# Kernel optimization log

Measured on AMD Instinct MI355X. Metric: run time of the kernel, lower is better.

## Reference

```python
import jax, jax.numpy as jnp
import numpy as np

G = (1.0, 1.0)  # Clifford signature g = [1, 1]
MODES1 = 32
MODES2 = 32


def _clifford_kernel_2d(w, g):
    # w: (4, O, Cin, 2*m1, 2*m2); returns (4*O, 4*Cin, 2*m1, 2*m2)
    g0, g1 = g
    k0 = jnp.concatenate([w[0], g0 * w[1], g1 * w[2], -g0 * g1 * w[3]], axis=1)
    k1 = jnp.concatenate([w[1], w[0], -g1 * w[3], g1 * w[2]], axis=1)
    k2 = jnp.concatenate([w[2], g0 * w[3], w[0], -g0 * w[1]], axis=1)
    k3 = jnp.concatenate([w[3], w[2], -w[1], w[0]], axis=1)
    return jnp.concatenate([k0, k1, k2, k3], axis=0)


def _forward(x, weights):
    # x: (B, C, H, W, 4) multivector field
    B, C, H, W, I = x.shape
    m1, m2 = MODES1, MODES2
    # dual-pair complexification: (scalar, e12) and (e1, e2)
    d1 = jax.lax.complex(x[..., 0], x[..., 3])
    d2 = jax.lax.complex(x[..., 1], x[..., 2])
    d1f = jnp.fft.fft2(d1)  # over last two axes (H, W)
    d2f = jnp.fft.fft2(d2)
    # stacked blades in Fourier space: (B, 4*C, H, W)
    mv = jnp.concatenate([d1f.real, d2f.real, d2f.imag, d1f.imag], axis=1)
    # crop low-frequency corner modes into a (2*m1, 2*m2) block
    top = jnp.concatenate([mv[:, :, :m1, :m2], mv[:, :, :m1, -m2:]], axis=-1)
    bot = jnp.concatenate([mv[:, :, -m1:, :m2], mv[:, :, -m1:, -m2:]], axis=-1)
    inp = jnp.concatenate([top, bot], axis=-2)  # (B, 4*C, 2*m1, 2*m2)
    kernel = _clifford_kernel_2d(weights, G)  # (4*O, 4*C, 2*m1, 2*m2)
    out = jnp.einsum('bixy,oixy->boxy', inp, kernel)  # geometric-product mode mix
    O4 = kernel.shape[0]
    # scatter the four corners back into a zero-padded full spectrum
    out_ft = jnp.zeros((B, O4, H, W), dtype=x.dtype)
    out_ft = out_ft.at[:, :, :m1, :m2].set(out[:, :, :m1, :m2])
    out_ft = out_ft.at[:, :, -m1:, :m2].set(out[:, :, -m1:, :m2])
    out_ft = out_ft.at[:, :, :m1, -m2:].set(out[:, :, :m1, -m2:])
    out_ft = out_ft.at[:, :, -m1:, -m2:].set(out[:, :, -m1:, -m2:])
    # (B, 4, O, H, W) -> (B, O, H, W, 4)
    out_ft = out_ft.reshape(B, 4, O4 // 4, H, W).transpose(0, 2, 3, 4, 1)
    od1 = jax.lax.complex(out_ft[..., 0], out_ft[..., 3])
    od2 = jax.lax.complex(out_ft[..., 1], out_ft[..., 2])
    o1 = jnp.fft.ifft2(od1)
    o2 = jnp.fft.ifft2(od2)
    return jnp.stack([o1.real, o2.real, o2.imag, o1.imag], axis=-1)


def setup_inputs() -> dict:
    key = jax.random.key(0)
    kx, kw = jax.random.split(key)
    B, Cin, Cout, H, W = 4, 32, 32, 256, 256
    x = jax.random.normal(kx, (B, Cin, H, W, 4), dtype=jnp.float32)
    scale = 1.0 / (Cin * Cout)
    weights = scale * jax.random.uniform(kw, (4, Cout, Cin, 2 * MODES1, 2 * MODES2), dtype=jnp.float32)
    return {"x": x, "weights": weights}


def reference(x, weights):
    return _forward(x, weights)
```

## Files before the change

### kernel.cpp

```cpp
#include <hip/hip_runtime.h>
#include <hip/hip_fp16.h>
#include <math.h>

#define TWO_PI 6.28318530717958647692f

__device__ __forceinline__ void cmac(float2& a, const float2 b, const float2 c) {
  a.x = fmaf(b.x, c.x, fmaf(-b.y, c.y, a.x));
  a.y = fmaf(b.x, c.y, fmaf(b.y, c.x, a.y));
}
__device__ __forceinline__ __half2 pkh(const float xx, const float yy) {
  return __floats2half2_rn(xx, yy);
}
__device__ __forceinline__ float2 uph(const __half2 h) { return __half22float2(h); }

#define FMA4(a, b, v)                 \
  {                                   \
    a.x = fmaf(b.x, v.x, a.x);        \
    a.y = fmaf(b.y, v.y, a.y);        \
    a.z = fmaf(b.z, v.z, a.z);        \
    a.w = fmaf(b.w, v.w, a.w);        \
  }
#define FMS4(a, b, v)                 \
  {                                   \
    a.x = fmaf(-b.x, v.x, a.x);       \
    a.y = fmaf(-b.y, v.y, a.y);       \
    a.z = fmaf(-b.z, v.z, a.z);       \
    a.w = fmaf(-b.w, v.w, a.w);       \
  }

#define W16_C {1.f, 0.92387953f, 0.70710678f, 0.38268343f, 0.f, -0.38268343f, -0.70710678f, -0.92387953f, -1.f, -0.92387953f, -0.70710678f, -0.38268343f, 0.f, 0.38268343f, 0.70710678f, 0.92387953f}
#define W16_S {0.f, 0.38268343f, 0.70710678f, 0.92387953f, 1.f, 0.92387953f, 0.70710678f, 0.38268343f, 0.f, -0.38268343f, -0.70710678f, -0.92387953f, -1.f, -0.92387953f, -0.70710678f, -0.38268343f}

__device__ __forceinline__ void idft16_p1(const float2* a, const int p1,
                                          float2* X) {
  const float WC[16] = W16_C;
  const float WS[16] = W16_S;
  float2 tt[4];
#pragma unroll
  for (int r1 = 0; r1 < 4; ++r1) {
    const float2 q0 = a[r1], q1 = a[r1 + 4], q2 = a[r1 + 8], q3 = a[r1 + 12];
    const float2 s = make_float2(q0.x + q2.x, q0.y + q2.y);
    const float2 d = make_float2(q0.x - q2.x, q0.y - q2.y);
    const float2 u = make_float2(q1.x + q3.x, q1.y + q3.y);
    const float2 e = make_float2(q1.x - q3.x, q1.y - q3.y);
    float2 in;
    if (p1 == 0)      in = make_float2(s.x + u.x, s.y + u.y);
    else if (p1 == 1) in = make_float2(d.x - e.y, d.y + e.x);
    else if (p1 == 2) in = make_float2(s.x - u.x, s.y - u.y);
    else              in = make_float2(d.x + e.y, d.y - e.x);
    const float wc = WC[(r1 * p1) & 15], ws = WS[(r1 * p1) & 15];
    tt[r1] = make_float2(fmaf(in.x, wc, -in.y * ws), fmaf(in.y, wc, in.x * ws));
  }
  const float2 s = make_float2(tt[0].x + tt[2].x, tt[0].y + tt[2].y);
  const float2 d = make_float2(tt[0].x - tt[2].x, tt[0].y - tt[2].y);
  const float2 u = make_float2(tt[1].x + tt[3].x, tt[1].y + tt[3].y);
  const float2 e = make_float2(tt[1].x - tt[3].x, tt[1].y - tt[3].y);
  X[0] = make_float2(s.x + u.x, s.y + u.y);
  X[1] = make_float2(d.x - e.y, d.y + e.x);
  X[2] = make_float2(s.x - u.x, s.y - u.y);
  X[3] = make_float2(d.x + e.y, d.y - e.x);
}

__global__ __launch_bounds__(512) void f1_dft_h(const float* __restrict__ x,
                                                __half2* __restrict__ G) {
  __shared__ float2 twn[256];
  __shared__ __align__(16) __half2 yf[64][4][17][2];
  const int t = threadIdx.x;
  if (t < 256) {
    float sv, cv;
    sincosf(-TWO_PI * (float)t * (1.0f / 256.0f), &sv, &cv);
    twn[t] = make_float2(cv, sv);
  }
  const int bid = blockIdx.x;
  const int img = bid >> 4;
  const int w0  = (bid & 15) << 4;
  const float4* __restrict__ xb = (const float4*)x + (size_t)img * 65536 + w0;
#pragma unroll
  for (int i = 0; i < 2; ++i) {
    const int idxs = t + (i << 9);
    const int n1 = idxs >> 4, wl = idxs & 15;
    const float4 v0 = xb[(size_t)(n1)*256 + wl];
    const float4 v1 = xb[(size_t)(n1 + 64) * 256 + wl];
    const float4 v2 = xb[(size_t)(n1 + 128) * 256 + wl];
    const float4 v3 = xb[(size_t)(n1 + 192) * 256 + wl];
    {
      const float sx = v0.x + v2.x, sy = v0.w + v2.w;
      const float dx = v0.x - v2.x, dy = v0.w - v2.w;
      const float ux = v1.x + v3.x, uy = v1.w + v3.w;
      const float ex = v1.x - v3.x, ey = v1.w - v3.w;
      yf[n1][0][wl][0] = pkh(sx + ux, sy + uy);
      yf[n1][2][wl][0] = pkh(sx - ux, sy - uy);
      yf[n1][1][wl][0] = pkh(dx + ey, dy - ex);
      yf[n1][3][wl][0] = pkh(dx - ey, dy + ex);
    }
    {
      const float sx = v0.y + v2.y, sy = v0.z + v2.z;
      const float dx = v0.y - v2.y, dy = v0.z - v2.z;
      const float ux = v1.y + v3.y, uy = v1.z + v3.z;
      const float ex = v1.y - v3.y, ey = v1.z - v3.z;
      yf[n1][0][wl][1] = pkh(sx + ux, sy + uy);
      yf[n1][2][wl][1] = pkh(sx - ux, sy - uy);
      yf[n1][1][wl][1] = pkh(dx + ey, dy - ex);
      yf[n1][3][wl][1] = pkh(dx - ey, dy + ex);
    }
  }
  __syncthreads();
  const int wl   = t & 15;
  const int dual = (t >> 4) & 1;
  const int kb   = t >> 5;
  const int r    = kb & 3;
  float2 a[16];
#pragma unroll
  for (int c = 0; c < 16; ++c) a[c] = make_float2(0.f, 0.f);
  int idx = 0;
#pragma unroll
  for (int n1 = 0; n1 < 64; ++n1) {
    const float2 tv = twn[idx];
    const float2 yv = uph(yf[n1][r][wl][dual]);
    cmac(a[n1 & 15], yv, tv);
    idx = (idx + kb) & 255;
  }
  const float WC[16] = W16_C;
  const float WS[16] = W16_S;
  float2 D0 = make_float2(0.f, 0.f), D1 = D0, D2 = D0, D3 = D0;
#pragma unroll
  for (int c = 0; c < 16; ++c) {
    const float2 av = a[c];
    const float cc = WC[c], ss = WS[c];
    const float cc2 = WC[(2 * c) & 15], ss2 = WS[(2 * c) & 15];
    D0.x += av.x;                        D0.y += av.y;
    D1.x = fmaf(av.x, cc,  fmaf( av.y, ss,  D1.x));
    D1.y = fmaf(av.y, cc,  fmaf(-av.x, ss,  D1.y));
    D2.x = fmaf(av.x, cc2, fmaf(-av.y, ss2, D2.x));
    D2.y = fmaf(av.y, cc2, fmaf( av.x, ss2, D2.y));
    D3.x = fmaf(av.x, cc,  fmaf(-av.y, ss,  D3.x));
    D3.y = fmaf(av.y, cc,  fmaf( av.x, ss,  D3.y));
  }
  __syncthreads();
  __half2(*dl)[64][16] = reinterpret_cast<__half2(*)[64][16]>(&yf[0][0][0][0]);
  dl[dual][kb][wl]      = pkh(D0.x, D0.y);
  dl[dual][kb + 16][wl] = pkh(D1.x, D1.y);
  dl[dual][kb + 32][wl] = pkh(D2.x, D2.y);
  dl[dual][kb + 48][wl] = pkh(D3.x, D3.y);
  __syncthreads();
  const __half2* __restrict__ dfl = &dl[0][0][0];
  const int flat = t << 2;
  const int wq = flat & 15, kx = (flat >> 4) & 63, dd = flat >> 10;
  const size_t row = (size_t)(img * 2 + dd) * 64 + kx;
  *reinterpret_cast<float4*>(&G[row * 256 + w0 + wq]) =
      *reinterpret_cast<const float4*>(&dfl[flat]);
}

__global__ __launch_bounds__(256) void f2_dft_w(const __half2* __restrict__ G,
                                                __half2* __restrict__ mi) {
  __shared__ float2 twn[256];
  __shared__ float2 yf[16][65][4];
  const int t = threadIdx.x;
  {
    float sv, cv;
    sincosf(-TWO_PI * (float)t * (1.0f / 256.0f), &sv, &cv);
    twn[t] = make_float2(cv, sv);
  }
  const int row0 = blockIdx.x * 16;
  for (int idx = t; idx < 1024; idx += 256) {
    const int tr = idx >> 6, n1 = idx & 63;
    const __half2* __restrict__ Gp = G + (size_t)(row0 + tr) * 256;
    const float2 z0 = uph(Gp[n1]), z1 = uph(Gp[n1 + 64]);
    const float2 z2 = uph(Gp[n1 + 128]), z3 = uph(Gp[n1 + 192]);
    const float sx = z0.x + z2.x, sy = z0.y + z2.y;
    const float dx = z0.x - z2.x, dy = z0.y - z2.y;
    const float ux = z1.x + z3.x, uy = z1.y + z3.y;
    const float ex = z1.x - z3.x, ey = z1.y - z3.y;
    yf[tr][n1][0] = make_float2(sx + ux, sy + uy);
    yf[tr][n1][2] = make_float2(sx - ux, sy - uy);
    yf[tr][n1][1] = make_float2(dx + ey, dy - ex);
    yf[tr][n1][3] = make_float2(dx - ey, dy + ex);
  }
  __syncthreads();
  const int kslot = t & 15;
  const int trow  = t >> 4;
  const int r     = kslot & 3;
  float2 acc[16];
#pragma unroll
  for (int c = 0; c < 16; ++c) acc[c] = make_float2(0.f, 0.f);
  int idx = 0;
#pragma unroll
  for (int n1 = 0; n1 < 64; ++n1) {
    const float2 tv = twn[idx];
    const float2 yv = yf[trow][n1][r];
    cmac(acc[n1 & 15], yv, tv);
    idx = (idx + kslot) & 255;
  }
  const float WC[16] = W16_C;
  const float WS[16] = W16_S;
  float2 D[4];
  D[0] = make_float2(0.f, 0.f); D[1] = D[0]; D[2] = D[0]; D[3] = D[0];
#pragma unroll
  for (int c = 0; c < 16; ++c) {
    const float2 a = acc[c];
    const float cc = WC[c], ss = WS[c];
    const float cc2 = WC[(2 * c) & 15], ss2 = WS[(2 * c) & 15];
    D[0].x += a.x;                        D[0].y += a.y;
    D[1].x = fmaf(a.x, cc,  fmaf( a.y, ss,  D[1].x));
    D[1].y = fmaf(a.y, cc,  fmaf(-a.x, ss,  D[1].y));
    D[2].x = fmaf(a.x, cc2, fmaf(-a.y, ss2, D[2].x));
    D[2].y = fmaf(a.y, cc2, fmaf( a.x, ss2, D[2].y));
    D[3].x = fmaf(a.x, cc,  fmaf(-a.y, ss,  D[3].x));
    D[3].y = fmaf(a.y, cc,  fmaf( a.x, ss,  D[3].y));
  }
  const int row  = row0 + trow;
  const int kx   = row & 63;
  const int dual = (row >> 6) & 1;
  const int bc   = row >> 7;
  const int b = bc >> 5, cc = bc & 31;
#pragma unroll
  for (int m = 0; m < 4; ++m) {
    const int kyi = kslot + (m << 4);
    mi[((size_t)((b * 2 + dual) * 32 + cc)) * 4096 + kx * 64 + kyi] =
        pkh(D[m].x, D[m].y);
  }
}

__global__ __launch_bounds__(256) void ein_k(const __half2* __restrict__ mi,
                                             const float* __restrict__ wgt,
                                             __half2* __restrict__ mo) {
  __shared__ float si[4][128][16];
  const int t = threadIdx.x;
  const int bid = blockIdx.x;
  const int m0 = (bid >> 1) << 4;
  const int oh = bid & 1;
  for (int idx = t; idx < 4096; idx += 256) {
    const int q = idx & 15, c = (idx >> 4) & 31, dual = (idx >> 9) & 1, b = idx >> 10;
    const float2 f = uph(mi[((size_t)((b * 2 + dual) * 32 + c)) * 4096 + m0 + q]);
    if (dual == 0) { si[b][c][q] = f.x;      si[b][96 + c][q] = f.y; }
    else           { si[b][32 + c][q] = f.x; si[b][64 + c][q] = f.y; }
  }
  __syncthreads();
  const int qv  = t & 3;
  const int o16 = (t >> 2) & 15;
  const int b   = t >> 6;
  const int o   = oh * 16 + o16;
  const int q0  = qv << 2;
  const float* __restrict__ wb = wgt + (size_t)o * 131072 + m0 + q0;
  float4 acc[4];
#pragma unroll
  for (int r = 0; r < 4; ++r) acc[r] = make_float4(0.f, 0.f, 0.f, 0.f);
  float4 wA[4], wB[4];
#pragma unroll
  for (int j = 0; j < 4; ++j)
    wA[j] = *reinterpret_cast<const float4*>(&wb[(size_t)j * 4194304]);
#pragma unroll
  for (int j = 0; j < 4; ++j)
    wB[j] = *reinterpret_cast<const float4*>(&wb[(size_t)j * 4194304 + 4096]);
#pragma unroll 1
  for (int c = 0; c < 32; ++c) {
    float4 wv[4];
#pragma unroll
    for (int j = 0; j < 4; ++j) { wv[j] = wA[j]; wA[j] = wB[j]; }
    if (c + 2 < 32) {
#pragma unroll
      for (int j = 0; j < 4; ++j)
        wB[j] = *reinterpret_cast<const float4*>(
            &wb[(size_t)j * 4194304 + (size_t)(c + 2) * 4096]);
    }
    const float4 iv0 = *reinterpret_cast<const float4*>(&si[b][c][q0]);
    const float4 iv1 = *reinterpret_cast<const float4*>(&si[b][32 + c][q0]);
    const float4 iv2 = *reinterpret_cast<const float4*>(&si[b][64 + c][q0]);
    const float4 iv3 = *reinterpret_cast<const float4*>(&si[b][96 + c][q0]);
    FMA4(acc[0], wv[0], iv0); FMA4(acc[0], wv[1], iv1);
    FMA4(acc[0], wv[2], iv2); FMS4(acc[0], wv[3], iv3);
    FMA4(acc[1], wv[1], iv0); FMA4(acc[1], wv[0], iv1);
    FMS4(acc[1], wv[3], iv2); FMA4(acc[1], wv[2], iv3);
    FMA4(acc[2], wv[2], iv0); FMA4(acc[2], wv[3], iv1);
    FMA4(acc[2], wv[0], iv2); FMS4(acc[2], wv[1], iv3);
    FMA4(acc[3], wv[3], iv0); FMA4(acc[3], wv[2], iv1);
    FMS4(acc[3], wv[1], iv2); FMA4(acc[3], wv[0], iv3);
  }
  __half2 h0[4], h1[4];
  h0[0] = pkh(acc[0].x, acc[3].x); h0[1] = pkh(acc[0].y, acc[3].y);
  h0[2] = pkh(acc[0].z, acc[3].z); h0[3] = pkh(acc[0].w, acc[3].w);
  h1[0] = pkh(acc[1].x, acc[2].x); h1[1] = pkh(acc[1].y, acc[2].y);
  h1[2] = pkh(acc[1].z, acc[2].z); h1[3] = pkh(acc[1].w, acc[2].w);
  *reinterpret_cast<float4*>(&mo[((size_t)((b * 2 + 0) * 32 + o)) * 4096 + m0 + q0]) =
      *reinterpret_cast<const float4*>(h0);
  *reinterpret_cast<float4*>(&mo[((size_t)((b * 2 + 1) * 32 + o)) * 4096 + m0 + q0]) =
      *reinterpret_cast<const float4*>(h1);
}

__global__ __launch_bounds__(256) void i1_idft_w(const __half2* __restrict__ mo,
                                                 __half2* __restrict__ T) {
  __shared__ float2 twc[256];
  __shared__ float2 srow[16][66];
  const int t = threadIdx.x;
  {
    float sv, cv;
    sincosf(TWO_PI * (float)t * (1.0f / 256.0f), &sv, &cv);
    twc[t] = make_float2(cv, sv);
  }
  const int row0 = blockIdx.x * 16;
  for (int idx = t; idx < 1024; idx += 256) {
    const int tr = idx >> 6, ky = idx & 63;
    const int row = row0 + tr;
    const int kx = row & 63;
    const int dual = (row >> 6) & 1;
    const int bo = row >> 7;
    const int b = bo >> 5, o = bo & 31;
    srow[tr][ky] =
        uph(mo[((size_t)((b * 2 + dual) * 32 + o)) * 4096 + kx * 64 + ky]);
  }
  __syncthreads();
  const int n1   = t & 15;
  const int trow = t >> 4;
  float2 a[16];
#pragma unroll
  for (int c = 0; c < 16; ++c) a[c] = make_float2(0.f, 0.f);
  int idx = 0;
#pragma unroll
  for (int kyi = 0; kyi < 64; ++kyi) {
    if (kyi == 32) idx = (idx + 192 * n1) & 255;
    cmac(a[kyi & 15], srow[trow][kyi], twc[idx]);
    idx = (idx + n1) & 255;
  }
  const int row = row0 + trow;
  __half2* __restrict__ Tp = T + (size_t)row * 256;
#pragma unroll
  for (int p1 = 0; p1 < 4; ++p1) {
    float2 X[4];
    idft16_p1(a, p1, X);
#pragma unroll
    for (int p2 = 0; p2 < 4; ++p2)
      Tp[n1 + 16 * (p1 + 4 * p2)] = pkh(X[p2].x, X[p2].y);
  }
}

__global__ __launch_bounds__(256) void i2_idft_h(const __half2* __restrict__ T,
                                                 float* __restrict__ out) {
  __shared__ float2 twc[256];
  __shared__ float2 Tl[2][64][16];
  const int t = threadIdx.x;
  {
    float sv, cv;
    sincosf(TWO_PI * (float)t * (1.0f / 256.0f), &sv, &cv);
    twc[t] = make_float2(cv, sv);
  }
  const int bid = blockIdx.x;
  const int bo = bid >> 4;
  const int w0 = (bid & 15) << 4;
  const __half2* __restrict__ Tp = T + (size_t)bo * 32768;
  for (int idx = t; idx < 2048; idx += 256) {
    const int ww = idx & 15, kxi = (idx >> 4) & 63, dual = idx >> 10;
    Tl[dual][kxi][ww] = uph(Tp[((size_t)dual * 64 + kxi) * 256 + w0 + ww]);
  }
  __syncthreads();
  const int wl = t & 15;
  const int n1 = t >> 4;
  float2 a0[16], a1[16];
#pragma unroll
  for (int c = 0; c < 16; ++c) {
    a0[c] = make_float2(0.f, 0.f);
    a1[c] = make_float2(0.f, 0.f);
  }
  int idx = 0;
#pragma unroll
  for (int kxi = 0; kxi < 64; ++kxi) {
    if (kxi == 32) idx = (idx + 192 * n1) & 255;
    const float2 tv = twc[idx];
    cmac(a0[kxi & 15], Tl[0][kxi][wl], tv);
    cmac(a1[kxi & 15], Tl[1][kxi][wl], tv);
    idx = (idx + n1) & 255;
  }
  const float sc = 1.0f / 65536.0f;
  float4* __restrict__ op = (float4*)out + (size_t)bo * 65536 + w0 + wl;
#pragma unroll
  for (int p1 = 0; p1 < 4; ++p1) {
    float2 X0[4], X1[4];
    idft16_p1(a0, p1, X0);
    idft16_p1(a1, p1, X1);
#pragma unroll
    for (int p2 = 0; p2 < 4; ++p2) {
      const int h = n1 + 16 * (p1 + 4 * p2);
      op[(size_t)h * 256] = make_float4(X0[p2].x * sc, X1[p2].x * sc,
                                        X1[p2].y * sc, X0[p2].y * sc);
    }
  }
}

extern "C" void kernel_launch(void* const* d_in, const int* in_sizes, int n_in,
                              void* d_out, int out_size, void* d_ws, size_t ws_size,
                              hipStream_t stream) {
  const float* x = (const float*)d_in[0];
  const float* wgt = (const float*)d_in[1];
  float* out = (float*)d_out;
  __half2* G  = (__half2*)d_ws;
  __half2* mi = G + 4194304;
  __half2* mo = mi + 1048576;

  hipLaunchKernelGGL(f1_dft_h, dim3(2048), dim3(512), 0, stream, x, G);
  hipLaunchKernelGGL(f2_dft_w, dim3(1024), dim3(256), 0, stream, G, mi);
  hipLaunchKernelGGL(ein_k,    dim3(512),  dim3(256), 0, stream, mi, wgt, mo);
  hipLaunchKernelGGL(i1_idft_w, dim3(1024), dim3(256), 0, stream, mo, G);
  hipLaunchKernelGGL(i2_idft_h, dim3(2048), dim3(256), 0, stream, G, out);
}
```

Baseline: 128.8 us.

## Split einsum over input channels so each weight load serves all batches

The mode-mixing kernel previously gave each thread one batch and all 32 input channels, so every weight was loaded from global memory four times, once per batch thread. Now each thread handles all four batches for a slice of 8 input channels, which cuts weight traffic fourfold. The partial sums are then combined through a shared-memory tree reduction. In exchange it uses 64 accumulator registers per thread, adds a large shared reduction buffer that lowers occupancy, and adds several barriers.

Measured after the change: 138.1 us. 1.07x slower.

```diff
diff --git a/kernel.cpp b/kernel.cpp
--- a/kernel.cpp
+++ b/kernel.cpp
@@ -59,6 +59,27 @@
   X[1] = make_float2(d.x - e.y, d.y + e.x);
   X[2] = make_float2(s.x - u.x, s.y - u.y);
   X[3] = make_float2(d.x + e.y, d.y - e.x);
+}
+
+__device__ __forceinline__ void clif_c(const float4 w[4],
+                                       const float (*si)[128][16],
+                                       const int c, const int q0,
+                                       float4 (*acc)[4]) {
+#pragma unroll
+  for (int b = 0; b < 4; ++b) {
+    const float4 iv0 = *reinterpret_cast<const float4*>(&si[b][c][q0]);
+    const float4 iv1 = *reinterpret_cast<const float4*>(&si[b][32 + c][q0]);
+    const float4 iv2 = *reinterpret_cast<const float4*>(&si[b][64 + c][q0]);
+    const float4 iv3 = *reinterpret_cast<const float4*>(&si[b][96 + c][q0]);
+    FMA4(acc[b][0], w[0], iv0); FMA4(acc[b][0], w[1], iv1);
+    FMA4(acc[b][0], w[2], iv2); FMS4(acc[b][0], w[3], iv3);
+    FMA4(acc[b][1], w[1], iv0); FMA4(acc[b][1], w[0], iv1);
+    FMS4(acc[b][1], w[3], iv2); FMA4(acc[b][1], w[2], iv3);
+    FMA4(acc[b][2], w[2], iv0); FMA4(acc[b][2], w[3], iv1);
+    FMA4(acc[b][2], w[0], iv2); FMS4(acc[b][2], w[1], iv3);
+    FMA4(acc[b][3], w[3], iv0); FMA4(acc[b][3], w[2], iv1);
+    FMS4(acc[b][3], w[1], iv2); FMA4(acc[b][3], w[0], iv3);
+  }
 }
 
 __global__ __launch_bounds__(512) void f1_dft_h(const float* __restrict__ x,
@@ -225,6 +246,7 @@
                                              const float* __restrict__ wgt,
                                              __half2* __restrict__ mo) {
   __shared__ float si[4][128][16];
+  __shared__ float red[128 * 65];
   const int t = threadIdx.x;
   const int bid = blockIdx.x;
   const int m0 = (bid >> 1) << 4;
@@ -236,55 +258,110 @@
     else           { si[b][32 + c][q] = f.x; si[b][64 + c][q] = f.y; }
   }
   __syncthreads();
-  const int qv  = t & 3;
+  const int qv = t & 3;
   const int o16 = (t >> 2) & 15;
-  const int b   = t >> 6;
-  const int o   = oh * 16 + o16;
-  const int q0  = qv << 2;
+  const int cs = t >> 6;
+  const int o = oh * 16 + o16;
+  const int q0 = qv << 2;
+  const int c0 = cs << 3;
   const float* __restrict__ wb = wgt + (size_t)o * 131072 + m0 + q0;
-  float4 acc[4];
-#pragma unroll
-  for (int r = 0; r < 4; ++r) acc[r] = make_float4(0.f, 0.f, 0.f, 0.f);
-  float4 wA[4], wB[4];
+  float4 acc[4][4];
+#pragma unroll
+  for (int b = 0; b < 4; ++b)
+#pragma unroll
+    for (int r = 0; r < 4; ++r) acc[b][r] = make_float4(0.f, 0.f, 0.f, 0.f);
+  float4 wE[4], wO[4];
 #pragma unroll
   for (int j = 0; j < 4; ++j)
-    wA[j] = *reinterpret_cast<const float4*>(&wb[(size_t)j * 4194304]);
+    wE[j] = *reinterpret_cast<const float4*>(&wb[(size_t)j * 4194304 + (size_t)c0 * 4096]);
 #pragma unroll
   for (int j = 0; j < 4; ++j)
-    wB[j] = *reinterpret_cast<const float4*>(&wb[(size_t)j * 4194304 + 4096]);
+    wO[j] = *reinterpret_cast<const float4*>(&wb[(size_t)j * 4194304 + (size_t)(c0 + 1) * 4096]);
 #pragma unroll 1
-  for (int c = 0; c < 32; ++c) {
-    float4 wv[4];
-#pragma unroll
-    for (int j = 0; j < 4; ++j) { wv[j] = wA[j]; wA[j] = wB[j]; }
-    if (c + 2 < 32) {
-#pragma unroll
-      for (int j = 0; j < 4; ++j)
-        wB[j] = *reinterpret_cast<const float4*>(
-            &wb[(size_t)j * 4194304 + (size_t)(c + 2) * 4096]);
-    }
-    const float4 iv0 = *reinterpret_cast<const float4*>(&si[b][c][q0]);
-    const float4 iv1 = *reinterpret_cast<const float4*>(&si[b][32 + c][q0]);
-    const float4 iv2 = *reinterpret_cast<const float4*>(&si[b][64 + c][q0]);
-    const float4 iv3 = *reinterpret_cast<const float4*>(&si[b][96 + c][q0]);
-    FMA4(acc[0], wv[0], iv0); FMA4(acc[0], wv[1], iv1);
-    FMA4(acc[0], wv[2], iv2); FMS4(acc[0], wv[3], iv3);
-    FMA4(acc[1], wv[1], iv0); FMA4(acc[1], wv[0], iv1);
-    FMS4(acc[1], wv[3], iv2); FMA4(acc[1], wv[2], iv3);
-    FMA4(acc[2], wv[2], iv0); FMA4(acc[2], wv[3], iv1);
-    FMA4(acc[2], wv[0], iv2); FMS4(acc[2], wv[1], iv3);
-    FMA4(acc[3], wv[3], iv0); FMA4(acc[3], wv[2], iv1);
-    FMS4(acc[3], wv[1], iv2); FMA4(acc[3], wv[0], iv3);
-  }
-  __half2 h0[4], h1[4];
-  h0[0] = pkh(acc[0].x, acc[3].x); h0[1] = pkh(acc[0].y, acc[3].y);
-  h0[2] = pkh(acc[0].z, acc[3].z); h0[3] = pkh(acc[0].w, acc[3].w);
-  h1[0] = pkh(acc[1].x, acc[2].x); h1[1] = pkh(acc[1].y, acc[2].y);
-  h1[2] = pkh(acc[1].z, acc[2].z); h1[3] = pkh(acc[1].w, acc[2].w);
-  *reinterpret_cast<float4*>(&mo[((size_t)((b * 2 + 0) * 32 + o)) * 4096 + m0 + q0]) =
-      *reinterpret_cast<const float4*>(h0);
-  *reinterpret_cast<float4*>(&mo[((size_t)((b * 2 + 1) * 32 + o)) * 4096 + m0 + q0]) =
-      *reinterpret_cast<const float4*>(h1);
+  for (int cc = 0; cc < 8; cc += 2) {
+    const int c = c0 + cc;
+    {
+      clif_c(wE, si, c, q0, acc);
+      if (cc + 2 < 8) {
+#pragma unroll
+        for (int j = 0; j < 4; ++j)
+          wE[j] = *reinterpret_cast<const float4*>(
+              &wb[(size_t)j * 4194304 + (size_t)(c + 2) * 4096]);
+      }
+    }
+    {
+      clif_c(wO, si, c + 1, q0, acc);
+      if (cc + 3 < 8) {
+#pragma unroll
+        for (int j = 0; j < 4; ++j)
+          wO[j] = *reinterpret_cast<const float4*>(
+              &wb[(size_t)j * 4194304 + (size_t)(c + 3) * 4096]);
+      }
+    }
+  }
+  __syncthreads();
+  if (cs >= 2) {
+    const int tt = t - 128;
+    float* rp = &red[tt * 65];
+#pragma unroll
+    for (int b = 0; b < 4; ++b)
+#pragma unroll
+      for (int r = 0; r < 4; ++r) {
+        const int k = (b * 4 + r) * 4;
+        rp[k] = acc[b][r].x; rp[k + 1] = acc[b][r].y;
+        rp[k + 2] = acc[b][r].z; rp[k + 3] = acc[b][r].w;
+      }
+  }
+  __syncthreads();
+  if (cs < 2) {
+    const float* rp = &red[t * 65];
+#pragma unroll
+    for (int b = 0; b < 4; ++b)
+#pragma unroll
+      for (int r = 0; r < 4; ++r) {
+        const int k = (b * 4 + r) * 4;
+        acc[b][r].x += rp[k];     acc[b][r].y += rp[k + 1];
+        acc[b][r].z += rp[k + 2]; acc[b][r].w += rp[k + 3];
+      }
+  }
+  __syncthreads();
+  if (cs == 1) {
+    float* rp = &red[(t - 64) * 65];
+#pragma unroll
+    for (int b = 0; b < 4; ++b)
+#pragma unroll
+      for (int r = 0; r < 4; ++r) {
+        const int k = (b * 4 + r) * 4;
+        rp[k] = acc[b][r].x; rp[k + 1] = acc[b][r].y;
+        rp[k + 2] = acc[b][r].z; rp[k + 3] = acc[b][r].w;
+      }
+  }
+  __syncthreads();
+  if (cs == 0) {
+    const float* rp = &red[t * 65];
+#pragma unroll
+    for (int b = 0; b < 4; ++b)
+#pragma unroll
+      for (int r = 0; r < 4; ++r) {
+        const int k = (b * 4 + r) * 4;
+        acc[b][r].x += rp[k];     acc[b][r].y += rp[k + 1];
+        acc[b][r].z += rp[k + 2]; acc[b][r].w += rp[k + 3];
+      }
+    __half2 h0[4], h1[4];
+#pragma unroll
+    for (int b = 0; b < 4; ++b) {
+      h0[0] = pkh(acc[b][0].x, acc[b][3].x); h0[1] = pkh(acc[b][0].y, acc[b][3].y);
+      h0[2] = pkh(acc[b][0].z, acc[b][3].z); h0[3] = pkh(acc[b][0].w, acc[b][3].w);
+      h1[0] = pkh(acc[b][1].x, acc[b][2].x); h1[1] = pkh(acc[b][1].y, acc[b][2].y);
+      h1[2] = pkh(acc[b][1].z, acc[b][2].z); h1[3] = pkh(acc[b][1].w, acc[b][2].w);
+      *reinterpret_cast<float4*>(
+          &mo[((size_t)((b * 2 + 0) * 32 + o)) * 4096 + m0 + q0]) =
+          *reinterpret_cast<const float4*>(h0);
+      *reinterpret_cast<float4*>(
+          &mo[((size_t)((b * 2 + 1) * 32 + o)) * 4096 + m0 + q0]) =
+          *reinterpret_cast<const float4*>(h1);
+    }
+  }
 }
 
 __global__ __launch_bounds__(256) void i1_idft_w(const __half2* __restrict__ mo,
```
